# Kernel tuning notes

Hardware: AMD Instinct MI355X
Metric: run time of the kernel (lower is better)

## Reference

```python
import jax, jax.numpy as jnp
import numpy as np

D_MODEL = 1024
D_STATE = 64
D_CONV = 4
EXPAND = 2
N_HEADS = 16
D_INNER = D_MODEL * EXPAND            # 2048
HEAD_DIM = D_INNER // N_HEADS         # 128
Z_DIM = D_INNER + 2 * D_STATE * N_HEADS + N_HEADS  # 4112
RMS_EPS = 1.1920928955078125e-07      # torch.finfo(float32).eps (RMSNorm default)


def setup_inputs() -> dict:
    key = jax.random.key(0)
    ks = jax.random.split(key, 6)
    s = 0.02
    u = jax.random.normal(ks[0], (2, 4096, D_MODEL), dtype=jnp.float32)
    W_in = jax.random.normal(ks[1], (D_MODEL, Z_DIM), dtype=jnp.float32) * s
    conv_w = jax.random.normal(ks[2], (D_INNER, D_CONV), dtype=jnp.float32) * s
    conv_b = jnp.zeros((D_INNER,), dtype=jnp.float32)
    delta_param = jnp.zeros((N_HEADS,), dtype=jnp.float32)
    W_gate = jax.random.normal(ks[3], (D_MODEL, D_INNER), dtype=jnp.float32) * s
    norm_w = jnp.ones((D_INNER,), dtype=jnp.float32)
    W_out = jax.random.normal(ks[4], (D_INNER, D_MODEL), dtype=jnp.float32) * s
    return {"u": u, "W_in": W_in, "conv_w": conv_w, "conv_b": conv_b,
            "delta_param": delta_param, "W_gate": W_gate, "norm_w": norm_w, "W_out": W_out}


def _ssm_scan(x, dt, B_mat, C_mat, delta_param):
    # x: (B,L,nh,dh); dt: (B,L,nh); B_mat,C_mat: (B,L,nh,ds)
    delta = jax.nn.softplus(dt + delta_param[None, None, :])
    a_bar = jnp.exp(-delta * jnp.abs(dt))            # (B,L,nh)
    Bsz, L, nh, dh = x.shape
    ds = B_mat.shape[-1]
    h0 = jnp.zeros((Bsz, nh, dh, ds), dtype=x.dtype)

    def step(h, inp):
        a_t, x_t, b_t, c_t = inp                     # (B,nh),(B,nh,dh),(B,nh,ds),(B,nh,ds)
        h = a_t[:, :, None, None] * h + x_t[..., None] * b_t[:, :, None, :]
        y_t = jnp.einsum('bhds,bhs->bhd', h, c_t)
        return h, y_t

    # move time to leading axis for scan
    xs = (jnp.moveaxis(a_bar, 1, 0), jnp.moveaxis(x, 1, 0),
          jnp.moveaxis(B_mat, 1, 0), jnp.moveaxis(C_mat, 1, 0))
    _, ys = jax.lax.scan(step, h0, xs)               # ys: (L,B,nh,dh)
    return jnp.moveaxis(ys, 0, 1)                    # (B,L,nh,dh)


def _forward(u, W_in, conv_w, conv_b, delta_param, W_gate, norm_w, W_out):
    B, L, _ = u.shape
    z = u @ W_in                                      # (B,L,Z_DIM)
    x = z[..., :D_INNER]
    o = D_INNER
    B_mat = z[..., o:o + D_STATE * N_HEADS].reshape(B, L, N_HEADS, D_STATE)
    o += D_STATE * N_HEADS
    C_mat = z[..., o:o + D_STATE * N_HEADS].reshape(B, L, N_HEADS, D_STATE)
    o += D_STATE * N_HEADS
    dt = z[..., o:o + N_HEADS]                        # (B,L,nh)

    # depthwise causal conv1d (kernel size D_CONV, left pad D_CONV-1)
    pad = D_CONV - 1
    xp = jnp.pad(x, ((0, 0), (pad, 0), (0, 0)))       # (B,L+pad,d_inner)
    x_conv = conv_b[None, None, :]
    for k in range(D_CONV):
        x_conv = x_conv + xp[:, k:k + L, :] * conv_w[None, None, :, k]
    x = jax.nn.silu(x_conv)

    x_ssm = x.reshape(B, L, N_HEADS, HEAD_DIM)
    y = _ssm_scan(x_ssm, dt, B_mat, C_mat, delta_param)
    y = y.reshape(B, L, D_INNER)

    gate = jax.nn.sigmoid(u @ W_gate)
    y = gate * y
    # RMSNorm
    y = y * jax.lax.rsqrt(jnp.mean(y * y, axis=-1, keepdims=True) + RMS_EPS) * norm_w
    return y @ W_out


def reference(u, W_in, conv_w, conv_b, delta_param, W_gate, norm_w, W_out):
    return _forward(u, W_in, conv_w, conv_b, delta_param, W_gate, norm_w, W_out)
```

## Files before the change

### kernel.cpp

```cpp
#include <hip/hip_runtime.h>

#define BATCH   2
#define LSEQ    4096
#define DMODEL  1024
#define DINNER  2048
#define NHEADS  16
#define DSTATE  64
#define HEADDIM 128
#define ZDIM    4112
#define BLROWS  (BATCH*LSEQ)
#define QCHUNK  64
#define NCHUNK  (LSEQ/QCHUNK)
#define UPAD    1088
#define GPAD    2112

#define AS1 __attribute__((address_space(1)))
#define AS3 __attribute__((address_space(3)))

typedef __bf16 bf16;
typedef __bf16 bf16x8 __attribute__((ext_vector_type(8)));
typedef __bf16 bf16x4 __attribute__((ext_vector_type(4)));
typedef float  f32x4  __attribute__((ext_vector_type(4)));

__device__ __forceinline__ int lds_elem(int row, int c)
{
    return (row >> 1) * 64 + (row & 1) * 32 + (((c ^ ((row >> 1) & 3)) & 3) << 3);
}

__global__ void cvt_pad_kernel(const float* __restrict__ in, bf16* __restrict__ out)
{
    int gid = blockIdx.x * 256 + threadIdx.x;
    int row = gid >> 8, c4 = (gid & 255) * 4;
    float4 v = *reinterpret_cast<const float4*>(in + (size_t)row * DMODEL + c4);
    bf16x4 o;
    o[0] = (bf16)v.x; o[1] = (bf16)v.y; o[2] = (bf16)v.z; o[3] = (bf16)v.w;
    *reinterpret_cast<bf16x4*>(out + (size_t)row * UPAD + c4) = o;
}

__global__ void transpose_cvt_kernel(const float* __restrict__ src, bf16* __restrict__ dst,
                                     int R, int C, int Cpad, int dstS)
{
    __shared__ float tile[32][33];
    int tx = threadIdx.x;
    int ty = threadIdx.y;
    int c0 = blockIdx.x * 32;
    int r0 = blockIdx.y * 32;
#pragma unroll
    for (int q = 0; q < 4; q++) {
        int r = r0 + ty + q * 8;
        int c = c0 + tx;
        float v = 0.f;
        if (r < R && c < C) v = src[(size_t)r * C + c];
        tile[ty + q * 8][tx] = v;
    }
    __syncthreads();
#pragma unroll
    for (int q = 0; q < 4; q++) {
        int oc = c0 + ty + q * 8;
        int orr = r0 + tx;
        if (oc < Cpad && orr < R)
            dst[(size_t)oc * dstS + orr] = (bf16)tile[tx][ty + q * 8];
    }
}

template<int NSLICE, int KROW, int MODE, int NBN>
__global__ __launch_bounds__(256) void gemm_db3_kernel(
    const bf16* __restrict__ A, const bf16* __restrict__ Bt,
    bf16* __restrict__ z, bf16* __restrict__ g, float* __restrict__ lab,
    const float* __restrict__ dparam, float* __restrict__ c32)
{
    constexpr int SLOTSZ = 256 * 32;
    __shared__ __align__(16) bf16 lds[3 * SLOTSZ];
    const int tid = threadIdx.x;
    const int lane = tid & 63, wid = tid >> 6;
    const int wm = (wid >> 1) * 64, wn = (wid & 1) * 64;
    const int lml = lane & 15, kc = lane >> 4;

    const int bid = blockIdx.x;
    const int xcd = bid & 7;
    const int idx = bid >> 3;
    const int bm = xcd * 8 + (idx & 7);
    const int bn = idx >> 3;

    const bf16* Abase = A + (size_t)(bm * 128) * KROW;
    const bf16* Bbase = Bt + (size_t)(bn * 128) * KROW;

#define STAGE8(pp) do {                                                                  \
    const int _p = (pp); const int _slot = _p % 3; const size_t _ko = (size_t)_p * 32;   \
    _Pragma("unroll") for (int it = 0; it < 4; ++it) {                                   \
        int q = it * 256 + tid;                                                          \
        int o = (q < 512) ? q : q - 512;                                                 \
        int prow = o >> 3, wi = o & 7;                                                   \
        int row = prow * 2 + (wi >> 2), c = (wi & 3) ^ (prow & 3);                       \
        const bf16* _src = ((q < 512) ? Abase : Bbase) + (size_t)row * KROW + _ko + c * 8; \
        int _dst = _slot * SLOTSZ + ((q < 512) ? 0 : 4096) + o * 8;                      \
        __builtin_amdgcn_global_load_lds((const AS1 void*)_src,                          \
            (AS3 void*)(&lds[_dst]), 16, 0, 0);                                          \
    }                                                                                    \
} while (0)

    f32x4 acc[4][4];
#pragma unroll
    for (int i = 0; i < 4; i++)
#pragma unroll
        for (int j = 0; j < 4; j++) acc[i][j] = (f32x4){0.f, 0.f, 0.f, 0.f};

    STAGE8(0); STAGE8(1); STAGE8(2);
    asm volatile("s_waitcnt vmcnt(8)" ::: "memory");
    __builtin_amdgcn_s_barrier();

    for (int p = 0; p < NSLICE; ++p) {
        const bf16* base_ = &lds[(p % 3) * SLOTSZ];
        bf16x8 af[4], bfv[4];
#pragma unroll
        for (int i = 0; i < 4; ++i) {
            int row = wm + i * 16 + lml;
            af[i] = *reinterpret_cast<const bf16x8*>(&base_[lds_elem(row, kc)]);
        }
#pragma unroll
        for (int j = 0; j < 4; ++j) {
            int row = wn + j * 16 + lml;
            bfv[j] = *reinterpret_cast<const bf16x8*>(&base_[4096 + lds_elem(row, kc)]);
        }
        asm volatile("s_waitcnt lgkmcnt(0)" ::: "memory");
        __builtin_amdgcn_sched_barrier(0);
        __builtin_amdgcn_s_barrier();
        if (p + 3 < NSLICE) STAGE8(p + 3);
#pragma unroll
        for (int i = 0; i < 4; ++i)
#pragma unroll
            for (int j = 0; j < 4; ++j)
                acc[i][j] = __builtin_amdgcn_mfma_f32_16x16x32_bf16(af[i], bfv[j], acc[i][j], 0, 0, 0);
        if (p + 1 < NSLICE) {
            if (p + 3 < NSLICE)       { asm volatile("s_waitcnt vmcnt(8)" ::: "memory"); }
            else if (p + 2 < NSLICE)  { asm volatile("s_waitcnt vmcnt(4)" ::: "memory"); }
            else                      { asm volatile("s_waitcnt vmcnt(0)" ::: "memory"); }
            __builtin_amdgcn_s_barrier();
        }
    }
#undef STAGE8

    const int rbase = (lane >> 4) * 4;
#pragma unroll
    for (int i = 0; i < 4; i++) {
#pragma unroll
        for (int j = 0; j < 4; j++) {
            int col = bn * 128 + wn + j * 16 + lml;
            if constexpr (MODE == 0) {
                bool isZ = (col < ZDIM);
                bool isG = (col >= 4224) && (col < 4224 + DINNER);
                bool isDT = (col >= 4096) && (col < ZDIM);
                if (!isZ && !isG) continue;
#pragma unroll
                for (int r = 0; r < 4; r++) {
                    int row = bm * 128 + wm + i * 16 + rbase + r;
                    float v = acc[i][j][r];
                    if (isZ) {
                        z[(size_t)row * ZDIM + col] = (bf16)v;
                        if (isDT) {
                            int h = col - 4096;
                            float v2 = v + dparam[h];
                            float sp = (v2 > 20.f) ? v2 : log1pf(expf(v2));
                            lab[(size_t)row * NHEADS + h] = -sp * fabsf(v);
                        }
                    } else {
                        g[(size_t)row * GPAD + (col - 4224)] = (bf16)v;
                    }
                }
            } else {
#pragma unroll
                for (int r = 0; r < 4; r++) {
                    int row = bm * 128 + wm + i * 16 + rbase + r;
                    c32[(size_t)row * 1024 + col] = acc[i][j][r];
                }
            }
        }
    }
}

__global__ __launch_bounds__(256) void chunk_state_kernel(
    const bf16* __restrict__ zz,
    const float* __restrict__ conv_w, const float* __restrict__ conv_b,
    const float* __restrict__ la,
    bf16* __restrict__ S,
    float* __restrict__ Adec)
{
    __shared__ __align__(16) bf16 xt[HEADDIM * QCHUNK];
    __shared__ __align__(16) bf16 bw[DSTATE * QCHUNK];
    __shared__ float Ls[QCHUNK];
    const int blk = blockIdx.x;
    const int h = blk & 15, c = (blk >> 4) & 63, b = blk >> 10;
    const int tid = threadIdx.x, lane = tid & 63, w = tid >> 6;
    const size_t row0 = (size_t)b * LSEQ + (size_t)c * QCHUNK;
    const bf16* zxg = zz + row0 * ZDIM + h * HEADDIM;
    const bf16* Bg  = zz + row0 * ZDIM + DINNER + h * DSTATE;

    const int tg = (tid >> 4) * 4;
    const int dg8 = (tid & 15) * 8;
    float wv[8][4], xa[4][8];
#pragma unroll
    for (int e = 0; e < 8; e++) {
        float4 w4 = *reinterpret_cast<const float4*>(conv_w + (size_t)(h * HEADDIM + dg8 + e) * 4);
        wv[e][0] = w4.x; wv[e][1] = w4.y; wv[e][2] = w4.z; wv[e][3] = w4.w;
        float bb = conv_b[h * HEADDIM + dg8 + e];
#pragma unroll
        for (int tt = 0; tt < 4; tt++) xa[tt][e] = bb;
    }
#pragma unroll
    for (int r = 0; r < 7; r++) {
        int lrow = c * QCHUNK + tg + r - 3;
        if (lrow >= 0) {
            bf16x8 zv = *reinterpret_cast<const bf16x8*>(zxg + (ptrdiff_t)(tg + r - 3) * ZDIM + dg8);
#pragma unroll
            for (int tt = 0; tt < 4; tt++) {
                int k = r - tt;
                if (k >= 0 && k < 4) {
#pragma unroll
                    for (int e = 0; e < 8; e++)
                        xa[tt][e] = fmaf((float)zv[e], wv[e][k], xa[tt][e]);
                }
            }
        }
    }
#pragma unroll
    for (int tt = 0; tt < 4; tt++)
#pragma unroll
        for (int e = 0; e < 8; e++)
            xa[tt][e] = xa[tt][e] / (1.f + expf(-xa[tt][e]));

    const int t = tid >> 2, sseg = (tid & 3) * 16;
    bf16x8 br[2];
#pragma unroll
    for (int q = 0; q < 2; q++)
        br[q] = *reinterpret_cast<const bf16x8*>(Bg + (size_t)t * ZDIM + sseg + q * 8);

    if (w == 0) {
        float v = la[(row0 + lane) * NHEADS + h];
#pragma unroll
        for (int off = 1; off < 64; off <<= 1) { float o = __shfl_up(v, off); if (lane >= off) v += o; }
        Ls[lane] = v;
        if (lane == 63) Adec[((size_t)b * NHEADS + h) * NCHUNK + c] = __expf(v);
    }
    __syncthreads();
    const float wt = __expf(Ls[QCHUNK - 1] - Ls[t]);
#pragma unroll
    for (int tt = 0; tt < 4; tt++) {
        int t2 = tg + tt;
#pragma unroll
        for (int e = 0; e < 8; e++) {
            int d = dg8 + e;
            xt[d * 64 + (((t2 >> 3) ^ (d & 7)) << 3) + (t2 & 7)] = (bf16)xa[tt][e];
        }
    }
    const int tb = t >> 3, ti = t & 7;
#pragma unroll
    for (int q = 0; q < 2; q++)
#pragma unroll
        for (int j = 0; j < 8; j++) {
            int s = sseg + q * 8 + j;
            bw[s * 64 + ((tb ^ (s & 7)) << 3) + ti] = (bf16)((float)br[q][j] * wt);
        }
    __syncthreads();

    f32x4 acc[2][4];
#pragma unroll
    for (int i = 0; i < 2; i++)
#pragma unroll
        for (int j = 0; j < 4; j++) acc[i][j] = (f32x4){0.f, 0.f, 0.f, 0.f};
#pragma unroll
    for (int kk = 0; kk < 2; kk++) {
        const int kb = kk * 4 + (lane >> 4);
        bf16x8 af[2], bf2[4];
#pragma unroll
        for (int i = 0; i < 2; i++) {
            int d = w * 32 + i * 16 + (lane & 15);
            af[i] = *reinterpret_cast<const bf16x8*>(&xt[d * 64 + ((kb ^ (d & 7)) << 3)]);
        }
#pragma unroll
        for (int j = 0; j < 4; j++) {
            int s = j * 16 + (lane & 15);
            bf2[j] = *reinterpret_cast<const bf16x8*>(&bw[s * 64 + ((kb ^ (s & 7)) << 3)]);
        }
#pragma unroll
        for (int i = 0; i < 2; i++)
#pragma unroll
            for (int j = 0; j < 4; j++)
                acc[i][j] = __builtin_amdgcn_mfma_f32_16x16x32_bf16(af[i], bf2[j], acc[i][j], 0, 0, 0);
    }
    bf16* Sg = S + ((size_t)(b * NCHUNK + c) * NHEADS + h) * (HEADDIM * DSTATE);
    const int rr = (lane >> 4) * 4, ccol = lane & 15;
#pragma unroll
    for (int i = 0; i < 2; i++)
#pragma unroll
        for (int j = 0; j < 4; j++)
#pragma unroll
            for (int r = 0; r < 4; r++)
                Sg[(w * 32 + i * 16 + rr + r) * 64 + j * 16 + ccol] = (bf16)acc[i][j][r];
}

__global__ void chunk_carry_kernel(bf16* S, const float* __restrict__ A)
{
    int gid = blockIdx.x * 256 + threadIdx.x;
    if (gid >= BATCH * NHEADS * HEADDIM * DSTATE) return;
    int es = gid & (HEADDIM * DSTATE - 1);
    int h  = (gid >> 13) & (NHEADS - 1);
    int b  = gid >> 17;
    const float* Ab = A + ((size_t)b * NHEADS + h) * NCHUNK;
    float hstate = 0.f;
    size_t stride = (size_t)NHEADS * HEADDIM * DSTATE;
    bf16* p = S + ((size_t)b * NCHUNK * NHEADS + h) * (HEADDIM * DSTATE) + es;
    for (int c = 0; c < NCHUNK; ++c) {
        float sv = (float)*p;
        *p = (bf16)hstate;
        hstate = fmaf(Ab[c], hstate, sv);
        p += stride;
    }
}

__global__ __launch_bounds__(256) void chunk_y_kernel(
    bf16* __restrict__ yout,
    const bf16* __restrict__ zz,
    const float* __restrict__ conv_w, const float* __restrict__ conv_b,
    const float* __restrict__ la,
    const bf16* __restrict__ H)
{
    __shared__ __align__(16) bf16 bc[QCHUNK * 128];
    __shared__ __align__(16) bf16 xt[HEADDIM * QCHUNK];
    __shared__ __align__(16) bf16 hl[HEADDIM * DSTATE];
    __shared__ float Ls[QCHUNK];
    const int blk = blockIdx.x;
    const int h = blk & 15, c = (blk >> 4) & 63, b = blk >> 10;
    const int tid = threadIdx.x, lane = tid & 63, w = tid >> 6;
    const size_t row0 = (size_t)b * LSEQ + (size_t)c * QCHUNK;
    bf16* yg = yout + row0 * DINNER + h * HEADDIM;
    const bf16* zxg = zz + row0 * ZDIM + h * HEADDIM;
    const bf16* Bg = zz + row0 * ZDIM + DINNER + h * DSTATE;
    const bf16* Cg = Bg + NHEADS * DSTATE;
    const bf16* Hg = H + ((size_t)(b * NCHUNK + c) * NHEADS + h) * (HEADDIM * DSTATE);

#pragma unroll
    for (int it = 0; it < 2; it++) {
        int idx = it * 256 + tid;
        int row = idx >> 3, p = idx & 7;
        int sc = (p ^ (row & 7)) << 3;
        __builtin_amdgcn_global_load_lds((const AS1 void*)(Bg + (size_t)row * ZDIM + sc),
                                         (AS3 void*)(&bc[idx * 8]), 16, 0, 0);
        __builtin_amdgcn_global_load_lds((const AS1 void*)(Cg + (size_t)row * ZDIM + sc),
                                         (AS3 void*)(&bc[4096 + idx * 8]), 16, 0, 0);
    }
#pragma unroll
    for (int it = 0; it < 4; it++) {
        int idx = it * 256 + tid;
        int d = idx >> 3, p = idx & 7;
        __builtin_amdgcn_global_load_lds((const AS1 void*)(Hg + d * 64 + ((p ^ (d & 7)) << 3)),
                                         (AS3 void*)(&hl[idx * 8]), 16, 0, 0);
    }

    const int tg = (tid >> 4) * 4;
    const int dg8 = (tid & 15) * 8;
    float wv[8][4], xa[4][8];
#pragma unroll
    for (int e = 0; e < 8; e++) {
        float4 w4 = *reinterpret_cast<const float4*>(conv_w + (size_t)(h * HEADDIM + dg8 + e) * 4);
        wv[e][0] = w4.x; wv[e][1] = w4.y; wv[e][2] = w4.z; wv[e][3] = w4.w;
        float bb = conv_b[h * HEADDIM + dg8 + e];
#pragma unroll
        for (int tt = 0; tt < 4; tt++) xa[tt][e] = bb;
    }
#pragma unroll
    for (int r = 0; r < 7; r++) {
        int lrow = c * QCHUNK + tg + r - 3;
        if (lrow >= 0) {
            bf16x8 zv = *reinterpret_cast<const bf16x8*>(zxg + (ptrdiff_t)(tg + r - 3) * ZDIM + dg8);
#pragma unroll
            for (int tt = 0; tt < 4; tt++) {
                int k = r - tt;
                if (k >= 0 && k < 4) {
#pragma unroll
                    for (int e = 0; e < 8; e++)
                        xa[tt][e] = fmaf((float)zv[e], wv[e][k], xa[tt][e]);
                }
            }
        }
    }
#pragma unroll
    for (int tt = 0; tt < 4; tt++)
#pragma unroll
        for (int e = 0; e < 8; e++)
            xa[tt][e] = xa[tt][e] / (1.f + expf(-xa[tt][e]));

    const int t = tid >> 2, sseg = (tid & 3) * 16;
    if (w == 0) {
        float v = la[(row0 + lane) * NHEADS + h];
#pragma unroll
        for (int off = 1; off < 64; off <<= 1) { float o = __shfl_up(v, off); if (lane >= off) v += o; }
        Ls[lane] = v;
    }
    __syncthreads();

#pragma unroll
    for (int tt = 0; tt < 4; tt++) {
        int t2 = tg + tt;
#pragma unroll
        for (int e = 0; e < 8; e++) {
            int d = dg8 + e;
            xt[d * 64 + (((t2 >> 3) ^ (d & 7)) << 3) + (t2 & 7)] = (bf16)xa[tt][e];
        }
    }

    f32x4 g[4];
#pragma unroll
    for (int j = 0; j < 4; j++) g[j] = (f32x4){0.f, 0.f, 0.f, 0.f};
#pragma unroll
    for (int kk = 0; kk < 2; kk++) {
        const int kb = kk * 4 + (lane >> 4);
        const int tA = w * 16 + (lane & 15);
        bf16x8 ca = *reinterpret_cast<const bf16x8*>(&bc[4096 + tA * 64 + ((kb ^ (tA & 7)) << 3)]);
#pragma unroll
        for (int j = 0; j < 4; j++) {
            int tB = j * 16 + (lane & 15);
            bf16x8 bb = *reinterpret_cast<const bf16x8*>(&bc[tB * 64 + ((kb ^ (tB & 7)) << 3)]);
            g[j] = __builtin_amdgcn_mfma_f32_16x16x32_bf16(ca, bb, g[j], 0, 0, 0);
        }
    }
    bf16x8 cr[2];
#pragma unroll
    for (int q = 0; q < 2; q++) {
        int sblk = (sseg >> 3) + q;
        cr[q] = *reinterpret_cast<const bf16x8*>(&bc[4096 + t * 64 + ((sblk ^ (t & 7)) << 3)]);
    }
    const float pscale = __expf(Ls[t]);
    __syncthreads();

    {
        const int tpbase = lane & 15;
        const int tgbase = w * 16 + (lane >> 4) * 4;
        float lst[4];
#pragma unroll
        for (int r = 0; r < 4; r++) lst[r] = Ls[tgbase + r];
#pragma unroll
        for (int j = 0; j < 4; j++) {
            int tp = j * 16 + tpbase;
            float lstp = Ls[tp];
#pragma unroll
            for (int r = 0; r < 4; r++) {
                int tg2 = tgbase + r;
                float mg = (tp <= tg2) ? g[j][r] * __expf(lst[r] - lstp) : 0.f;
                bc[tg2 * 128 + (((tp >> 3) ^ (tg2 & 7)) << 3) + (tp & 7)] = (bf16)mg;
            }
        }
    }
#pragma unroll
    for (int q = 0; q < 2; q++) {
        int sblk = (sseg >> 3) + q;
        bf16x8 o;
#pragma unroll
        for (int j = 0; j < 8; j++) o[j] = (bf16)((float)cr[q][j] * pscale);
        *reinterpret_cast<bf16x8*>(&bc[t * 128 + ((8 + (sblk ^ (t & 7))) << 3)]) = o;
    }
    __syncthreads();

    f32x4 acc[2][4];
#pragma unroll
    for (int i = 0; i < 2; i++)
#pragma unroll
        for (int j = 0; j < 4; j++) acc[i][j] = (f32x4){0.f, 0.f, 0.f, 0.f};
#pragma unroll
    for (int kk = 0; kk < 4; kk++) {
        const int kb = kk * 4 + (lane >> 4);
        bf16x8 af[2];
#pragma unroll
        for (int i = 0; i < 2; i++) {
            int d = w * 32 + i * 16 + (lane & 15);
            if (kk < 2)
                af[i] = *reinterpret_cast<const bf16x8*>(&xt[d * 64 + ((kb ^ (d & 7)) << 3)]);
            else
                af[i] = *reinterpret_cast<const bf16x8*>(&hl[d * 64 + (((kb - 8) ^ (d & 7)) << 3)]);
        }
#pragma unroll
        for (int j = 0; j < 4; j++) {
            int tt = j * 16 + (lane & 15);
            bf16x8 b2 = *reinterpret_cast<const bf16x8*>(&bc[tt * 128 + ((kb ^ (tt & 7)) << 3)]);
#pragma unroll
            for (int i = 0; i < 2; i++)
                acc[i][j] = __builtin_amdgcn_mfma_f32_16x16x32_bf16(af[i], b2, acc[i][j], 0, 0, 0);
        }
    }
#pragma unroll
    for (int i = 0; i < 2; i++)
#pragma unroll
        for (int j = 0; j < 4; j++) {
            int d0 = w * 32 + i * 16 + (lane >> 4) * 4;
            int tt = j * 16 + (lane & 15);
            bf16x4 o;
#pragma unroll
            for (int r = 0; r < 4; r++) o[r] = (bf16)acc[i][j][r];
            *reinterpret_cast<bf16x4*>(yg + (size_t)tt * DINNER + d0) = o;
        }
}

__global__ __launch_bounds__(256) void gate_rms_kernel(
    const bf16* __restrict__ y,
    bf16* g,
    const float* __restrict__ norm_w)
{
    __shared__ float red[4];
    int row = blockIdx.x, t = threadIdx.x;
    const bf16* yr = y + (size_t)row * DINNER;
    bf16* gr = g + (size_t)row * GPAD;
    int c0 = t * 8;
    bf16x8 yv8 = *reinterpret_cast<const bf16x8*>(yr + c0);
    bf16x8 gv8 = *reinterpret_cast<const bf16x8*>(gr + c0);
    float v[8];
#pragma unroll
    for (int i = 0; i < 8; i++) {
        float yf = (float)yv8[i];
        float gf = (float)gv8[i];
        v[i] = yf / (1.f + expf(-gf));
    }
    float ss = 0.f;
#pragma unroll
    for (int i = 0; i < 8; i++) ss += v[i] * v[i];
#pragma unroll
    for (int off = 32; off >= 1; off >>= 1) ss += __shfl_xor(ss, off);
    if ((t & 63) == 0) red[t >> 6] = ss;
    __syncthreads();
    ss = red[0] + red[1] + red[2] + red[3];
    float sc = rsqrtf(ss * (1.0f / DINNER) + 1.1920928955078125e-07f);
    float4 na = *reinterpret_cast<const float4*>(norm_w + c0);
    float4 nb = *reinterpret_cast<const float4*>(norm_w + c0 + 4);
    bf16x8 ov;
    ov[0] = (bf16)(v[0] * sc * na.x);
    ov[1] = (bf16)(v[1] * sc * na.y);
    ov[2] = (bf16)(v[2] * sc * na.z);
    ov[3] = (bf16)(v[3] * sc * na.w);
    ov[4] = (bf16)(v[4] * sc * nb.x);
    ov[5] = (bf16)(v[5] * sc * nb.y);
    ov[6] = (bf16)(v[6] * sc * nb.z);
    ov[7] = (bf16)(v[7] * sc * nb.w);
    *reinterpret_cast<bf16x8*>(gr + c0) = ov;
}

extern "C" void kernel_launch(void* const* d_in, const int* in_sizes, int n_in,
                              void* d_out, int out_size, void* d_ws, size_t ws_size,
                              hipStream_t stream)
{
    const float* u      = (const float*)d_in[0];
    const float* W_in   = (const float*)d_in[1];
    const float* conv_w = (const float*)d_in[2];
    const float* conv_b = (const float*)d_in[3];
    const float* dparam = (const float*)d_in[4];
    const float* W_gate = (const float*)d_in[5];
    const float* norm_w = (const float*)d_in[6];
    const float* W_out  = (const float*)d_in[7];
    float* out = (float*)d_out;

    char* ws = (char*)d_ws;
    size_t off = 0;
    auto alloc = [&](size_t bytes) {
        void* p = ws + off;
        off += (bytes + 255) & ~(size_t)255;
        return p;
    };
    bf16*  u_bf  = (bf16*) alloc((size_t)BLROWS * UPAD * 2);
    bf16*  Wt_f  = (bf16*) alloc((size_t)6400 * UPAD * 2);
    bf16*  Wt_o  = (bf16*) alloc((size_t)DMODEL * GPAD * 2);
    bf16*  z     = (bf16*) alloc((size_t)BLROWS * ZDIM * 2);
    bf16*  g     = (bf16*) alloc((size_t)BLROWS * GPAD * 2);
    float* lab   = (float*)alloc((size_t)BLROWS * NHEADS * 4);
    bf16*  S     = (bf16*) alloc((size_t)BATCH * NCHUNK * NHEADS * HEADDIM * DSTATE * 2);
    float* Adec  = (float*)alloc((size_t)BATCH * NHEADS * NCHUNK * 4);
    bf16* xy = (bf16*)d_out;
    (void)ws_size; (void)in_sizes; (void)n_in; (void)out_size;

    dim3 tb(32, 8);
    cvt_pad_kernel<<<BLROWS, 256, 0, stream>>>(u, u_bf);
    transpose_cvt_kernel<<<dim3(4224 / 32, DMODEL / 32), tb, 0, stream>>>(W_in, Wt_f, DMODEL, ZDIM, 4224, UPAD);
    transpose_cvt_kernel<<<dim3(2176 / 32, DMODEL / 32), tb, 0, stream>>>(W_gate, Wt_f + (size_t)4224 * UPAD, DMODEL, DINNER, 2176, UPAD);
    transpose_cvt_kernel<<<dim3(DMODEL / 32, DINNER / 32), tb, 0, stream>>>(W_out, Wt_o, DINNER, DMODEL, DMODEL, GPAD);

    gemm_db3_kernel<32, UPAD, 0, 50><<<64 * 50, 256, 0, stream>>>(
        u_bf, Wt_f, z, g, lab, dparam, nullptr);

    chunk_state_kernel<<<BATCH * NCHUNK * NHEADS, 256, 0, stream>>>(z, conv_w, conv_b, lab, S, Adec);
    chunk_carry_kernel<<<(BATCH * NHEADS * HEADDIM * DSTATE) / 256, 256, 0, stream>>>(S, Adec);
    chunk_y_kernel<<<BATCH * NCHUNK * NHEADS, 256, 0, stream>>>(xy, z, conv_w, conv_b, lab, S);

    gate_rms_kernel<<<BLROWS, 256, 0, stream>>>(xy, g, norm_w);

    gemm_db3_kernel<64, GPAD, 1, 8><<<64 * 8, 256, 0, stream>>>(
        g, Wt_o, nullptr, nullptr, nullptr, nullptr, out);
}
```

Before: 331.4 us.

## Fuse gating and RMSNorm into chunk_y and defer row scaling to output GEMM

The chunk_y kernel now applies the sigmoid gate itself, writes the gated values straight into the g buffer, and emits per-head partial sums of squares. A tiny kernel reduces these into per-row RMS scales, which the output GEMM epilogue applies. norm_w is folded into the transposed W_out weights. This removes the separate gate_rms pass and the y intermediate round trip through memory, at the cost of an extra psum buffer, a small reduction kernel, and applying the norm scale after bf16 rounding of the unnormalized values.

```diff
diff --git a/kernel.cpp b/kernel.cpp
--- a/kernel.cpp
+++ b/kernel.cpp
@@ -38,7 +38,8 @@
 }
 
 __global__ void transpose_cvt_kernel(const float* __restrict__ src, bf16* __restrict__ dst,
-                                     int R, int C, int Cpad, int dstS)
+                                     int R, int C, int Cpad, int dstS,
+                                     const float* __restrict__ rowscale)
 {
     __shared__ float tile[32][33];
     int tx = threadIdx.x;
@@ -54,12 +55,14 @@
         tile[ty + q * 8][tx] = v;
     }
     __syncthreads();
+    float sc = 1.f;
+    if (rowscale && (r0 + tx) < R) sc = rowscale[r0 + tx];
 #pragma unroll
     for (int q = 0; q < 4; q++) {
         int oc = c0 + ty + q * 8;
         int orr = r0 + tx;
         if (oc < Cpad && orr < R)
-            dst[(size_t)oc * dstS + orr] = (bf16)tile[tx][ty + q * 8];
+            dst[(size_t)oc * dstS + orr] = (bf16)(tile[tx][ty + q * 8] * sc);
     }
 }
 
@@ -67,7 +70,7 @@
 __global__ __launch_bounds__(256) void gemm_db3_kernel(
     const bf16* __restrict__ A, const bf16* __restrict__ Bt,
     bf16* __restrict__ z, bf16* __restrict__ g, float* __restrict__ lab,
-    const float* __restrict__ dparam, float* __restrict__ c32)
+    const float* __restrict__ dparam, const float* __restrict__ rs, float* __restrict__ c32)
 {
     constexpr int SLOTSZ = 256 * 32;
     __shared__ __align__(16) bf16 lds[3 * SLOTSZ];
@@ -168,11 +171,12 @@
                     }
                 }
             } else {
-#pragma unroll
-                for (int r = 0; r < 4; r++) {
-                    int row = bm * 128 + wm + i * 16 + rbase + r;
-                    c32[(size_t)row * 1024 + col] = acc[i][j][r];
-                }
+                int row0 = bm * 128 + wm + i * 16 + rbase;
+                float4 rsv = *reinterpret_cast<const float4*>(rs + row0);
+                const float* rp = reinterpret_cast<const float*>(&rsv);
+#pragma unroll
+                for (int r = 0; r < 4; r++)
+                    c32[(size_t)(row0 + r) * 1024 + col] = acc[i][j][r] * rp[r];
             }
         }
     }
@@ -318,21 +322,23 @@
 }
 
 __global__ __launch_bounds__(256) void chunk_y_kernel(
-    bf16* __restrict__ yout,
+    bf16* __restrict__ gv,
     const bf16* __restrict__ zz,
     const float* __restrict__ conv_w, const float* __restrict__ conv_b,
     const float* __restrict__ la,
-    const bf16* __restrict__ H)
+    const bf16* __restrict__ H,
+    float* __restrict__ psum)
 {
     __shared__ __align__(16) bf16 bc[QCHUNK * 128];
     __shared__ __align__(16) bf16 xt[HEADDIM * QCHUNK];
     __shared__ __align__(16) bf16 hl[HEADDIM * DSTATE];
     __shared__ float Ls[QCHUNK];
+    __shared__ float wsum[4][QCHUNK];
     const int blk = blockIdx.x;
     const int h = blk & 15, c = (blk >> 4) & 63, b = blk >> 10;
     const int tid = threadIdx.x, lane = tid & 63, w = tid >> 6;
     const size_t row0 = (size_t)b * LSEQ + (size_t)c * QCHUNK;
-    bf16* yg = yout + row0 * DINNER + h * HEADDIM;
+    bf16* gg = gv + row0 * GPAD + h * HEADDIM;
     const bf16* zxg = zz + row0 * ZDIM + h * HEADDIM;
     const bf16* Bg = zz + row0 * ZDIM + DINNER + h * DSTATE;
     const bf16* Cg = Bg + NHEADS * DSTATE;
@@ -486,59 +492,49 @@
                 acc[i][j] = __builtin_amdgcn_mfma_f32_16x16x32_bf16(af[i], b2, acc[i][j], 0, 0, 0);
         }
     }
+
+    float ps[4] = {0.f, 0.f, 0.f, 0.f};
 #pragma unroll
     for (int i = 0; i < 2; i++)
 #pragma unroll
         for (int j = 0; j < 4; j++) {
             int d0 = w * 32 + i * 16 + (lane >> 4) * 4;
             int tt = j * 16 + (lane & 15);
+            bf16x4 gt = *reinterpret_cast<const bf16x4*>(gg + (size_t)tt * GPAD + d0);
             bf16x4 o;
 #pragma unroll
-            for (int r = 0; r < 4; r++) o[r] = (bf16)acc[i][j][r];
-            *reinterpret_cast<bf16x4*>(yg + (size_t)tt * DINNER + d0) = o;
-        }
-}
-
-__global__ __launch_bounds__(256) void gate_rms_kernel(
-    const bf16* __restrict__ y,
-    bf16* g,
-    const float* __restrict__ norm_w)
-{
-    __shared__ float red[4];
-    int row = blockIdx.x, t = threadIdx.x;
-    const bf16* yr = y + (size_t)row * DINNER;
-    bf16* gr = g + (size_t)row * GPAD;
-    int c0 = t * 8;
-    bf16x8 yv8 = *reinterpret_cast<const bf16x8*>(yr + c0);
-    bf16x8 gv8 = *reinterpret_cast<const bf16x8*>(gr + c0);
-    float v[8];
-#pragma unroll
-    for (int i = 0; i < 8; i++) {
-        float yf = (float)yv8[i];
-        float gf = (float)gv8[i];
-        v[i] = yf / (1.f + expf(-gf));
-    }
-    float ss = 0.f;
-#pragma unroll
-    for (int i = 0; i < 8; i++) ss += v[i] * v[i];
-#pragma unroll
-    for (int off = 32; off >= 1; off >>= 1) ss += __shfl_xor(ss, off);
-    if ((t & 63) == 0) red[t >> 6] = ss;
-    __syncthreads();
-    ss = red[0] + red[1] + red[2] + red[3];
-    float sc = rsqrtf(ss * (1.0f / DINNER) + 1.1920928955078125e-07f);
-    float4 na = *reinterpret_cast<const float4*>(norm_w + c0);
-    float4 nb = *reinterpret_cast<const float4*>(norm_w + c0 + 4);
-    bf16x8 ov;
-    ov[0] = (bf16)(v[0] * sc * na.x);
-    ov[1] = (bf16)(v[1] * sc * na.y);
-    ov[2] = (bf16)(v[2] * sc * na.z);
-    ov[3] = (bf16)(v[3] * sc * na.w);
-    ov[4] = (bf16)(v[4] * sc * nb.x);
-    ov[5] = (bf16)(v[5] * sc * nb.y);
-    ov[6] = (bf16)(v[6] * sc * nb.z);
-    ov[7] = (bf16)(v[7] * sc * nb.w);
-    *reinterpret_cast<bf16x8*>(gr + c0) = ov;
+            for (int r = 0; r < 4; r++) {
+                float gf = (float)gt[r];
+                float vv = acc[i][j][r] / (1.f + expf(-gf));
+                o[r] = (bf16)vv;
+                ps[j] = fmaf(vv, vv, ps[j]);
+            }
+            *reinterpret_cast<bf16x4*>(gg + (size_t)tt * GPAD + d0) = o;
+        }
+#pragma unroll
+    for (int j = 0; j < 4; j++) {
+        ps[j] += __shfl_xor(ps[j], 16);
+        ps[j] += __shfl_xor(ps[j], 32);
+    }
+    if ((lane >> 4) == 0) {
+#pragma unroll
+        for (int j = 0; j < 4; j++) wsum[w][j * 16 + (lane & 15)] = ps[j];
+    }
+    __syncthreads();
+    if (tid < QCHUNK) {
+        float tot = wsum[0][tid] + wsum[1][tid] + wsum[2][tid] + wsum[3][tid];
+        psum[(row0 + tid) * NHEADS + h] = tot;
+    }
+}
+
+__global__ void rowscale_kernel(const float* __restrict__ psum, float* __restrict__ rs)
+{
+    int r = blockIdx.x * 256 + threadIdx.x;
+    if (r >= BLROWS) return;
+    float s = 0.f;
+#pragma unroll
+    for (int h = 0; h < NHEADS; h++) s += psum[(size_t)r * NHEADS + h];
+    rs[r] = rsqrtf(s * (1.0f / DINNER) + 1.1920928955078125e-07f);
 }
 
 extern "C" void kernel_launch(void* const* d_in, const int* in_sizes, int n_in,
@@ -570,24 +566,25 @@
     float* lab   = (float*)alloc((size_t)BLROWS * NHEADS * 4);
     bf16*  S     = (bf16*) alloc((size_t)BATCH * NCHUNK * NHEADS * HEADDIM * DSTATE * 2);
     float* Adec  = (float*)alloc((size_t)BATCH * NHEADS * NCHUNK * 4);
-    bf16* xy = (bf16*)d_out;
+    float* psum  = (float*)alloc((size_t)BLROWS * NHEADS * 4);
+    float* rs    = (float*)alloc((size_t)BLROWS * 4);
     (void)ws_size; (void)in_sizes; (void)n_in; (void)out_size;
 
     dim3 tb(32, 8);
     cvt_pad_kernel<<<BLROWS, 256, 0, stream>>>(u, u_bf);
-    transpose_cvt_kernel<<<dim3(4224 / 32, DMODEL / 32), tb, 0, stream>>>(W_in, Wt_f, DMODEL, ZDIM, 4224, UPAD);
-    transpose_cvt_kernel<<<dim3(2176 / 32, DMODEL / 32), tb, 0, stream>>>(W_gate, Wt_f + (size_t)4224 * UPAD, DMODEL, DINNER, 2176, UPAD);
-    transpose_cvt_kernel<<<dim3(DMODEL / 32, DINNER / 32), tb, 0, stream>>>(W_out, Wt_o, DINNER, DMODEL, DMODEL, GPAD);
+    transpose_cvt_kernel<<<dim3(4224 / 32, DMODEL / 32), tb, 0, stream>>>(W_in, Wt_f, DMODEL, ZDIM, 4224, UPAD, nullptr);
+    transpose_cvt_kernel<<<dim3(2176 / 32, DMODEL / 32), tb, 0, stream>>>(W_gate, Wt_f + (size_t)4224 * UPAD, DMODEL, DINNER, 2176, UPAD, nullptr);
+    transpose_cvt_kernel<<<dim3(DMODEL / 32, DINNER / 32), tb, 0, stream>>>(W_out, Wt_o, DINNER, DMODEL, DMODEL, GPAD, norm_w);
 
     gemm_db3_kernel<32, UPAD, 0, 50><<<64 * 50, 256, 0, stream>>>(
-        u_bf, Wt_f, z, g, lab, dparam, nullptr);
+        u_bf, Wt_f, z, g, lab, dparam, nullptr, nullptr);
 
     chunk_state_kernel<<<BATCH * NCHUNK * NHEADS, 256, 0, stream>>>(z, conv_w, conv_b, lab, S, Adec);
     chunk_carry_kernel<<<(BATCH * NHEADS * HEADDIM * DSTATE) / 256, 256, 0, stream>>>(S, Adec);
-    chunk_y_kernel<<<BATCH * NCHUNK * NHEADS, 256, 0, stream>>>(xy, z, conv_w, conv_b, lab, S);
-
-    gate_rms_kernel<<<BLROWS, 256, 0, stream>>>(xy, g, norm_w);
+    chunk_y_kernel<<<BATCH * NCHUNK * NHEADS, 256, 0, stream>>>(g, z, conv_w, conv_b, lab, S, psum);
+
+    rowscale_kernel<<<(BLROWS + 255) / 256, 256, 0, stream>>>(psum, rs);
 
     gemm_db3_kernel<64, GPAD, 1, 8><<<64 * 8, 256, 0, stream>>>(
-        g, Wt_o, nullptr, nullptr, nullptr, nullptr, out);
-}
+        g, Wt_o, nullptr, nullptr, nullptr, nullptr, rs, out);
+}
```

New measurement: 321.7 us. 1.03x faster.
